# Optimization experiments

Measured on AMD Instinct MI355X. Metric: run time of the kernel, lower is better.

## Reference

```python
import jax, jax.numpy as jnp
import numpy as np

NUM_HEADS = 4
HEAD_DIM = 64
BN_EPS = 1e-5


def setup_inputs() -> dict:
    key = jax.random.key(0)
    ks = jax.random.split(key, 6)
    B, C, H, W = 8, 256, 48, 48
    HD = NUM_HEADS * HEAD_DIM  # 256
    x = jax.random.normal(ks[0], (B, C, H, W), dtype=jnp.float32)
    q_w = jax.random.normal(ks[1], (HD, C), dtype=jnp.float32) * (1.0 / np.sqrt(C))
    k_w = jax.random.normal(ks[2], (HEAD_DIM, C), dtype=jnp.float32) * (1.0 / np.sqrt(C))
    v_w = jax.random.normal(ks[3], (HEAD_DIM, C), dtype=jnp.float32) * (1.0 / np.sqrt(C))
    proj_w = jax.random.normal(ks[4], (C, HD), dtype=jnp.float32) * (1.0 / np.sqrt(HD))
    proj_b = jnp.zeros((C,), dtype=jnp.float32)
    gamma = jnp.ones((C,), dtype=jnp.float32)
    beta = jnp.zeros((C,), dtype=jnp.float32)
    return {"x": x, "q_w": q_w, "k_w": k_w, "v_w": v_w,
            "proj_w": proj_w, "proj_b": proj_b, "gamma": gamma, "beta": beta}


def reference(x, q_w, k_w, v_w, proj_w, proj_b, gamma, beta):
    B, C, H, W = x.shape
    N = H * W
    scale = HEAD_DIM ** -0.5
    xf = x.reshape(B, C, N)  # 1x1 conv == channel matmul
    q = jnp.einsum('oc,bcn->bon', q_w, xf).reshape(B, NUM_HEADS, HEAD_DIM, N)
    k = jnp.einsum('dc,bcn->bdn', k_w, xf)  # shared single KV head (MQA)
    v = jnp.einsum('dc,bcn->bdn', v_w, xf)
    # scores: [B, heads, N, N]
    attn = jnp.einsum('bhdn,bdm->bhnm', q, k) * scale
    attn = jax.nn.softmax(attn, axis=-1)
    out = jnp.einsum('bhnm,bdm->bhdn', attn, v)  # [B, heads, d, N]
    out = out.reshape(B, NUM_HEADS * HEAD_DIM, N)
    out = jnp.einsum('co,bon->bcn', proj_w, out) + proj_b[None, :, None]
    out = out.reshape(B, C, H, W)
    # BatchNorm2d (training-mode batch statistics, biased variance)
    mean = jnp.mean(out, axis=(0, 2, 3), keepdims=True)
    var = jnp.var(out, axis=(0, 2, 3), keepdims=True)
    out = gamma[None, :, None, None] * (out - mean) * jax.lax.rsqrt(var + BN_EPS) + beta[None, :, None, None]
    return out + x
```

## Files before the change

### kernel.cpp

```cpp
#include <hip/hip_runtime.h>
#include <hip/hip_bf16.h>
#include <math.h>

#define BB 8
#define CCH 256
#define NN 2304
#define NH 4
#define HDIM 64
#define QKV_ROWS 384
#define BN_EPS 1e-5f
#define NTILES 36
#define NPART 288
#define SLOG2E 0.18033688011112042f

typedef short bf16x8 __attribute__((ext_vector_type(8)));
typedef short bf16x4 __attribute__((ext_vector_type(4)));
typedef float f32x4 __attribute__((ext_vector_type(4)));

#if __has_builtin(__builtin_amdgcn_exp2f)
#define EXP2(x) __builtin_amdgcn_exp2f(x)
#else
#define EXP2(x) __expf((x) * 0.6931471805599453f)
#endif

#define MFMA32(a, b, c) __builtin_amdgcn_mfma_f32_16x16x32_bf16(a, b, c, 0, 0, 0)

__device__ __forceinline__ unsigned bfpair(float a, float b) {
    __hip_bfloat162 h = __float22bfloat162_rn(make_float2(a, b));
    return *(unsigned*)&h;
}
__device__ __forceinline__ unsigned short f2bf(float f) {
    unsigned u = __float_as_uint(f);
    u = (u + 0x7FFFu + ((u >> 16) & 1u)) >> 16;
    return (unsigned short)u;
}
__device__ __forceinline__ float bf2f(unsigned short s) {
    return __uint_as_float((unsigned)s << 16);
}

__global__ __launch_bounds__(256) void prep_k(
    const float* __restrict__ x,
    const float* __restrict__ qw, const float* __restrict__ kw,
    const float* __restrict__ vw, const float* __restrict__ pw,
    unsigned short* __restrict__ xT, unsigned short* __restrict__ xb,
    unsigned short* __restrict__ Wb, unsigned short* __restrict__ Pb)
{
    const int bid = blockIdx.x;
    const int tid = threadIdx.x;
    if (bid < 1152) {
        __shared__ float sX[64][65];
        const int b  = bid / 144;
        const int rem = bid - b * 144;
        const int nb = (rem >> 2) * 64;
        const int cb = (rem & 3) * 64;

        #pragma unroll
        for (int u = 0; u < 4; ++u) {
            int c  = (tid >> 4) + 16 * u;
            int n4 = (tid & 15) * 4;
            float4 v = *(const float4*)(x + ((size_t)(b * CCH + cb + c)) * NN + nb + n4);
            sX[c][n4+0] = v.x; sX[c][n4+1] = v.y; sX[c][n4+2] = v.z; sX[c][n4+3] = v.w;
        }
        __syncthreads();

        const int n  = tid >> 2;
        const int cg = (tid & 3) * 16;
        unsigned vals[8];
        #pragma unroll
        for (int p = 0; p < 8; ++p)
            vals[p] = bfpair(sX[cg + 2*p][n], sX[cg + 2*p + 1][n]);
        unsigned short* dst = xT + ((size_t)(b * NN + nb + n)) * CCH + cb + cg;
        *(uint4*)dst = make_uint4(vals[0], vals[1], vals[2], vals[3]);
        *(uint4*)(dst + 8) = make_uint4(vals[4], vals[5], vals[6], vals[7]);

        #pragma unroll
        for (int it = 0; it < 2; ++it) {
            int flat = tid + 256 * it;
            int row = flat >> 3;
            int n8  = (flat & 7) * 8;
            unsigned vv[4];
            #pragma unroll
            for (int p = 0; p < 4; ++p)
                vv[p] = bfpair(sX[row][n8 + 2*p], sX[row][n8 + 2*p + 1]);
            *(uint4*)(xb + ((size_t)(b * CCH + cb + row)) * NN + nb + n8) =
                make_uint4(vv[0], vv[1], vv[2], vv[3]);
        }
    } else {
        int idx = (bid - 1152) * 256 + tid;
        if (idx < 98304) {
            int o = idx >> 8, c = idx & 255;
            float v;
            if (o < 256)      v = qw[(size_t)o * CCH + c] * SLOG2E;
            else if (o < 320) v = kw[(size_t)(o - 256) * CCH + c];
            else              v = vw[(size_t)(o - 320) * CCH + c];
            Wb[idx] = f2bf(v);
        } else {
            int j = idx - 98304;
            if (j < 65536) Pb[j] = f2bf(pw[j]);
        }
    }
}

__global__ __launch_bounds__(128) void qkv_mfma_k(
    const unsigned short* __restrict__ Wb, const unsigned short* __restrict__ xT,
    unsigned short* __restrict__ Qt, unsigned short* __restrict__ Kt,
    unsigned short* __restrict__ Vn)
{
    __shared__ unsigned short sE[2][64 * 72];
    const int tid = threadIdx.x;
    const int wave = tid >> 6;
    const int lane = tid & 63;
    const int quad = lane >> 4;
    const int l15  = lane & 15;
    const int b  = blockIdx.x;
    const int nb = blockIdx.y * 64;
    const int mb = blockIdx.z * 128 + wave * 64;

    const unsigned short* Ab = Wb + (size_t)(mb + l15) * CCH + quad * 8;
    const unsigned short* Bb = xT + ((size_t)(b * NN + nb + l15)) * CCH + quad * 8;

    f32x4 C[4][4] = {};
    bf16x8 aA[2][4], bB[2][4];
    #pragma unroll
    for (int i = 0; i < 4; ++i) aA[0][i] = *(const bf16x8*)(Ab + (size_t)(16*i) * CCH);
    #pragma unroll
    for (int j = 0; j < 4; ++j) bB[0][j] = *(const bf16x8*)(Bb + (size_t)(16*j) * CCH);

    #pragma unroll
    for (int kk = 0; kk < 8; ++kk) {
        const int cur = kk & 1;
        if (kk < 7) {
            const int k1 = (kk + 1) * 32;
            #pragma unroll
            for (int i = 0; i < 4; ++i) aA[cur^1][i] = *(const bf16x8*)(Ab + (size_t)(16*i) * CCH + k1);
            #pragma unroll
            for (int j = 0; j < 4; ++j) bB[cur^1][j] = *(const bf16x8*)(Bb + (size_t)(16*j) * CCH + k1);
        }
        #pragma unroll
        for (int i = 0; i < 4; ++i)
            #pragma unroll
            for (int j = 0; j < 4; ++j)
                C[i][j] = MFMA32(aA[cur][i], bB[cur][j], C[i][j]);
    }

    unsigned short* sEw = &sE[wave][0];
    if (mb < 320) {
        #pragma unroll
        for (int i = 0; i < 4; ++i)
            #pragma unroll
            for (int j = 0; j < 4; ++j) {
                unsigned p01 = bfpair(C[i][j][0], C[i][j][1]);
                unsigned p23 = bfpair(C[i][j][2], C[i][j][3]);
                unsigned short* p = sEw + (16*j + l15) * 72 + 16*i + quad*4;
                *(unsigned*)p = p01;
                *(unsigned*)(p + 2) = p23;
            }
        if (mb < 256) {
            #pragma unroll
            for (int it = 0; it < 8; ++it) {
                int flat = lane + 64 * it;
                int row = flat >> 3;
                int o8  = (flat & 7) * 8;
                uint4 v = *(const uint4*)(sEw + row * 72 + o8);
                *(uint4*)(Qt + ((size_t)(b * NN + nb + row)) * CCH + mb + o8) = v;
            }
        } else {
            #pragma unroll
            for (int it = 0; it < 8; ++it) {
                int flat = lane + 64 * it;
                int row = flat >> 3;
                int o8  = (flat & 7) * 8;
                uint4 v = *(const uint4*)(sEw + row * 72 + o8);
                *(uint4*)(Kt + ((size_t)(b * NN + nb + row)) * 64 + o8) = v;
            }
        }
    } else {
        #pragma unroll
        for (int i = 0; i < 4; ++i)
            #pragma unroll
            for (int j = 0; j < 4; ++j) {
                unsigned p01 = bfpair(C[i][j][0], C[i][j][1]);
                unsigned p23 = bfpair(C[i][j][2], C[i][j][3]);
                unsigned short* p = sEw + (16*i + quad*4) * 72 + 16*j + l15;
                p[0]   = (unsigned short)p01;
                p[72]  = (unsigned short)(p01 >> 16);
                p[144] = (unsigned short)p23;
                p[216] = (unsigned short)(p23 >> 16);
            }
        #pragma unroll
        for (int it = 0; it < 8; ++it) {
            int flat = lane + 64 * it;
            int row = flat >> 3;
            int n8  = (flat & 7) * 8;
            uint4 v = *(const uint4*)(sEw + row * 72 + n8);
            *(uint4*)(Vn + ((size_t)(b * 64 + (mb - 320) + row)) * NN + nb + n8) = v;
        }
    }
}

__global__ __launch_bounds__(512, 8) void attn_k(
    const unsigned short* __restrict__ Qt,
    const unsigned short* __restrict__ Kt,
    const unsigned short* __restrict__ Vn,
    unsigned short* __restrict__ Ao)
{
    __shared__ __align__(16) unsigned short sKV[2 * 2 * 64 * 64];

    const int tid   = threadIdx.x;
    const int wave  = tid >> 6;
    const int lane  = tid & 63;
    const int quad  = lane >> 4;
    const int l15   = lane & 15;
    const int qslot = wave & 3;
    const int hloc  = wave >> 2;
    const int qoff  = qslot * 16;
    const int b     = blockIdx.x;
    const int nb    = blockIdx.y * 64;
    const int head  = blockIdx.z * 2 + hloc;

    const bf16x8 vone8 = {(short)0x3F80, (short)0x3F80, (short)0x3F80, (short)0x3F80,
                          (short)0x3F80, (short)0x3F80, (short)0x3F80, (short)0x3F80};

    bf16x8 bQ[2];
    const unsigned short* QtB = Qt + ((size_t)(b * NN + nb + qoff + l15)) * CCH + head * 64 + quad * 8;
    #pragma unroll
    for (int s = 0; s < 2; ++s)
        bQ[s] = *(const bf16x8*)(QtB + s * 32);

    const int srow = tid >> 3;
    const int swch = ((tid & 7) ^ (srow & 7)) * 8;
    const int krow = (srow & 3) | (((srow >> 3) & 3) << 2) | (((srow >> 2) & 1) << 4) | (srow & 32);
    const int kwch = ((tid & 7) ^ (krow & 7)) * 8;
    const int sgc8 = (tid & 7) * 8;

    bf16x8 pf[2];
    pf[0] = *(const bf16x8*)(Kt + ((size_t)(b * NN + srow)) * 64 + sgc8);
    pf[1] = *(const bf16x8*)(Vn + ((size_t)(b * 64 + srow)) * NN + sgc8);
    *(bf16x8*)(sKV + 0 * 4096 + krow * 64 + kwch) = pf[0];
    *(bf16x8*)(sKV + 1 * 4096 + srow * 64 + swch) = pf[1];
    pf[0] = *(const bf16x8*)(Kt + ((size_t)(b * NN + 64 + srow)) * 64 + sgc8);
    pf[1] = *(const bf16x8*)(Vn + ((size_t)(b * 64 + srow)) * NN + 64 + sgc8);

    f32x4 O[4] = {};
    f32x4 dacc = {};

    for (int step = 0; step < NTILES; ++step) {
        const int cur = step & 1;
        __syncthreads();

        if (step + 1 < NTILES) {
            unsigned short* dstb = sKV + (cur ^ 1) * 8192;
            *(bf16x8*)(dstb + 0 * 4096 + krow * 64 + kwch) = pf[0];
            *(bf16x8*)(dstb + 1 * 4096 + srow * 64 + swch) = pf[1];
        }
        if (step + 2 < NTILES) {
            const int keys0 = (step + 2) * 64;
            pf[0] = *(const bf16x8*)(Kt + ((size_t)(b * NN + keys0 + srow)) * 64 + sgc8);
            pf[1] = *(const bf16x8*)(Vn + ((size_t)(b * 64 + srow)) * NN + keys0 + sgc8);
        }

        const unsigned short* sKb = sKV + cur * 8192;
        const unsigned short* sVb = sKb + 4096;

        f32x4 C[4] = {};
        #pragma unroll
        for (int s = 0; s < 2; ++s)
            #pragma unroll
            for (int kt = 0; kt < 4; ++kt) {
                const int row = 16*kt + l15;
                const int chsw = ((s*4 + quad) ^ (row & 7)) * 8;
                bf16x8 aK = *(const bf16x8*)(sKb + row * 64 + chsw);
                C[kt] = MFMA32(aK, bQ[s], C[kt]);
            }

        bf16x8 bP[2];
        #pragma unroll
        for (int kt2 = 0; kt2 < 2; ++kt2) {
            union { unsigned u[4]; bf16x8 v; } xp;
            const f32x4 c0 = C[2*kt2];
            const f32x4 c1 = C[2*kt2+1];
            xp.u[0] = bfpair(EXP2(c0[0]), EXP2(c0[1]));
            xp.u[1] = bfpair(EXP2(c0[2]), EXP2(c0[3]));
            xp.u[2] = bfpair(EXP2(c1[0]), EXP2(c1[1]));
            xp.u[3] = bfpair(EXP2(c1[2]), EXP2(c1[3]));
            bP[kt2] = xp.v;
        }

        dacc = MFMA32(vone8, bP[0], dacc);
        dacc = MFMA32(vone8, bP[1], dacc);

        #pragma unroll
        for (int jd = 0; jd < 4; ++jd)
            #pragma unroll
            for (int kt2 = 0; kt2 < 2; ++kt2) {
                const int row = 16*jd + l15;
                const int chsw = ((4*kt2 + quad) ^ (row & 7)) * 8;
                bf16x8 aV = *(const bf16x8*)(sVb + row * 64 + chsw);
                O[jd] = MFMA32(aV, bP[kt2], O[jd]);
            }
    }
    __syncthreads();

    const float rinv = 1.0f / dacc[0];
    unsigned short* sT = (unsigned short*)sKV;
    #pragma unroll
    for (int jd = 0; jd < 4; ++jd) {
        unsigned lo = bfpair(O[jd][0] * rinv, O[jd][1] * rinv);
        unsigned hi = bfpair(O[jd][2] * rinv, O[jd][3] * rinv);
        *(uint2*)(sT + (hloc * 64 + qoff + l15) * 72 + 16*jd + quad*4) = make_uint2(lo, hi);
    }
    __syncthreads();

    #pragma unroll
    for (int it = 0; it < 2; ++it) {
        int flat = tid + 512 * it;
        int hh   = flat >> 9;
        int row  = (flat >> 3) & 63;
        int c8   = (flat & 7) * 8;
        uint4 v = *(const uint4*)(sT + (hh * 64 + row) * 72 + c8);
        *(uint4*)(Ao + ((size_t)(b * NN + nb + row)) * CCH + (blockIdx.z * 2 + hh) * 64 + c8) = v;
    }
}

__global__ __launch_bounds__(128) void proj_mfma_k(
    const unsigned short* __restrict__ Pb, const unsigned short* __restrict__ Ao,
    const float* __restrict__ pb, unsigned short* __restrict__ projb,
    float* __restrict__ psum, float* __restrict__ psq)
{
    __shared__ unsigned short sE[2][64 * 72];
    const int tid = threadIdx.x;
    const int wave = tid >> 6;
    const int lane = tid & 63;
    const int quad = lane >> 4;
    const int l15  = lane & 15;
    const int b  = blockIdx.x;
    const int nb = blockIdx.y * 64;
    const int mb = blockIdx.z * 128 + wave * 64;
    const int part = b * NTILES + blockIdx.y;

    const unsigned short* Ab = Pb + (size_t)(mb + l15) * CCH + quad * 8;
    const unsigned short* Bb = Ao + ((size_t)(b * NN + nb + l15)) * CCH + quad * 8;

    f32x4 C[4][4] = {};
    bf16x8 aA[2][4], bB[2][4];
    #pragma unroll
    for (int i = 0; i < 4; ++i) aA[0][i] = *(const bf16x8*)(Ab + (size_t)(16*i) * CCH);
    #pragma unroll
    for (int j = 0; j < 4; ++j) bB[0][j] = *(const bf16x8*)(Bb + (size_t)(16*j) * CCH);

    #pragma unroll
    for (int kk = 0; kk < 8; ++kk) {
        const int cur = kk & 1;
        if (kk < 7) {
            const int k1 = (kk + 1) * 32;
            #pragma unroll
            for (int i = 0; i < 4; ++i) aA[cur^1][i] = *(const bf16x8*)(Ab + (size_t)(16*i) * CCH + k1);
            #pragma unroll
            for (int j = 0; j < 4; ++j) bB[cur^1][j] = *(const bf16x8*)(Bb + (size_t)(16*j) * CCH + k1);
        }
        #pragma unroll
        for (int i = 0; i < 4; ++i)
            #pragma unroll
            for (int j = 0; j < 4; ++j)
                C[i][j] = MFMA32(aA[cur][i], bB[cur][j], C[i][j]);
    }

    unsigned short* sEw = &sE[wave][0];
    #pragma unroll
    for (int i = 0; i < 4; ++i) {
        #pragma unroll
        for (int r = 0; r < 4; ++r) {
            const int ch = mb + 16*i + quad*4 + r;
            const float bias = pb[ch];
            float v0 = C[i][0][r] + bias, v1 = C[i][1][r] + bias;
            float v2 = C[i][2][r] + bias, v3 = C[i][3][r] + bias;
            C[i][0][r] = v0; C[i][1][r] = v1; C[i][2][r] = v2; C[i][3][r] = v3;
            float rs = (v0 + v1) + (v2 + v3);
            float rq = (v0*v0 + v1*v1) + (v2*v2 + v3*v3);
            rs += __shfl_xor(rs, 1); rq += __shfl_xor(rq, 1);
            rs += __shfl_xor(rs, 2); rq += __shfl_xor(rq, 2);
            rs += __shfl_xor(rs, 4); rq += __shfl_xor(rq, 4);
            rs += __shfl_xor(rs, 8); rq += __shfl_xor(rq, 8);
            if (l15 == 0) {
                psum[(size_t)ch * NPART + part] = rs;
                psq [(size_t)ch * NPART + part] = rq;
            }
        }
    }

    #pragma unroll
    for (int i = 0; i < 4; ++i)
        #pragma unroll
        for (int j = 0; j < 4; ++j) {
            unsigned p01 = bfpair(C[i][j][0], C[i][j][1]);
            unsigned p23 = bfpair(C[i][j][2], C[i][j][3]);
            unsigned short* p = sEw + (16*i + quad*4) * 72 + 16*j + l15;
            p[0]   = (unsigned short)p01;
            p[72]  = (unsigned short)(p01 >> 16);
            p[144] = (unsigned short)p23;
            p[216] = (unsigned short)(p23 >> 16);
        }
    #pragma unroll
    for (int it = 0; it < 8; ++it) {
        int flat = lane + 64 * it;
        int row = flat >> 3;
        int n8  = (flat & 7) * 8;
        uint4 v = *(const uint4*)(sEw + row * 72 + n8);
        *(uint4*)(projb + ((size_t)(b * CCH + mb + row)) * NN + nb + n8) = v;
    }
}

__global__ __launch_bounds__(256) void bn_apply_k(
    const unsigned short* __restrict__ projb, const unsigned short* __restrict__ xb,
    const float* __restrict__ psum, const float* __restrict__ psq,
    const float* __restrict__ gamma, const float* __restrict__ beta,
    float* __restrict__ out)
{
    const int tid = threadIdx.x;
    const int b = blockIdx.x;
    const int c = blockIdx.y;

    float s = 0.f, q = 0.f;
    for (int k = tid; k < NPART; k += 256) {
        s += psum[(size_t)c * NPART + k];
        q += psq [(size_t)c * NPART + k];
    }
    __shared__ float rs[256], rq[256];
    rs[tid] = s; rq[tid] = q;
    __syncthreads();
    for (int off = 128; off > 0; off >>= 1) {
        if (tid < off) { rs[tid] += rs[tid + off]; rq[tid] += rq[tid + off]; }
        __syncthreads();
    }
    const float inv_n = 1.0f / (float)(BB * NN);
    float mean = rs[0] * inv_n;
    float var  = rq[0] * inv_n - mean * mean;
    float scv = gamma[c] * rsqrtf(var + BN_EPS);
    float shv = beta[c] - mean * scv;

    #pragma unroll
    for (int it = 0; it < 2; ++it) {
        int chunk = tid + 256 * it;
        if (chunk < 288) {
            size_t base = ((size_t)(b * CCH + c)) * NN + chunk * 8;
            uint4 pv = *(const uint4*)(projb + base);
            uint4 xv = *(const uint4*)(xb + base);
            const unsigned short* pp = (const unsigned short*)&pv;
            const unsigned short* xx = (const unsigned short*)&xv;
            float4 r0, r1;
            r0.x = scv * bf2f(pp[0]) + shv + bf2f(xx[0]);
            r0.y = scv * bf2f(pp[1]) + shv + bf2f(xx[1]);
            r0.z = scv * bf2f(pp[2]) + shv + bf2f(xx[2]);
            r0.w = scv * bf2f(pp[3]) + shv + bf2f(xx[3]);
            r1.x = scv * bf2f(pp[4]) + shv + bf2f(xx[4]);
            r1.y = scv * bf2f(pp[5]) + shv + bf2f(xx[5]);
            r1.z = scv * bf2f(pp[6]) + shv + bf2f(xx[6]);
            r1.w = scv * bf2f(pp[7]) + shv + bf2f(xx[7]);
            *(float4*)(out + base) = r0;
            *(float4*)(out + base + 4) = r1;
        }
    }
}

extern "C" void kernel_launch(void* const* d_in, const int* in_sizes, int n_in,
                              void* d_out, int out_size, void* d_ws, size_t ws_size,
                              hipStream_t stream)
{
    const float* x     = (const float*)d_in[0];
    const float* qw    = (const float*)d_in[1];
    const float* kw    = (const float*)d_in[2];
    const float* vw    = (const float*)d_in[3];
    const float* pw    = (const float*)d_in[4];
    const float* pb    = (const float*)d_in[5];
    const float* gamma = (const float*)d_in[6];
    const float* beta  = (const float*)d_in[7];
    float* out = (float*)d_out;

    char* ws = (char*)d_ws;
    unsigned short* xT = (unsigned short*)ws;
    unsigned short* Ao = (unsigned short*)ws;
    unsigned short* Wb = (unsigned short*)(ws + 9437184);
    unsigned short* Pb = (unsigned short*)(ws + 9633792);
    unsigned short* Qt = (unsigned short*)(ws + 9764864);
    unsigned short* Kt = (unsigned short*)(ws + 19202048);
    unsigned short* Vn = (unsigned short*)(ws + 21561344);
    unsigned short* projb = (unsigned short*)(ws + 9764864);
    float* psum  = (float*)(ws + 28639232);
    float* psq   = (float*)(ws + 28934144);
    unsigned short* xb = (unsigned short*)(ws + 29229056);

    prep_k<<<1792, 256, 0, stream>>>(x, qw, kw, vw, pw, xT, xb, Wb, Pb);

    dim3 g1(BB, NN / 64, 3);
    qkv_mfma_k<<<g1, 128, 0, stream>>>(Wb, xT, Qt, Kt, Vn);

    dim3 g2(BB, NN / 64, NH / 2);
    attn_k<<<g2, 512, 0, stream>>>(Qt, Kt, Vn, Ao);

    dim3 g3(BB, NN / 64, 2);
    proj_mfma_k<<<g3, 128, 0, stream>>>(Pb, Ao, pb, projb, psum, psq);

    dim3 g4(BB, CCH);
    bn_apply_k<<<g4, 256, 0, stream>>>(projb, xb, psum, psq, gamma, beta, out);
}
```

Baseline: 198.6 us.

## Give each attention wave two query tiles to reuse K/V fragments

```diff
diff --git a/kernel.cpp b/kernel.cpp
--- a/kernel.cpp
+++ b/kernel.cpp
@@ -198,7 +198,7 @@
     }
 }
 
-__global__ __launch_bounds__(512, 8) void attn_k(
+__global__ __launch_bounds__(256, 4) void attn_k(
     const unsigned short* __restrict__ Qt,
     const unsigned short* __restrict__ Kt,
     const unsigned short* __restrict__ Vn,
@@ -211,38 +211,47 @@
     const int lane  = tid & 63;
     const int quad  = lane >> 4;
     const int l15   = lane & 15;
-    const int qslot = wave & 3;
-    const int hloc  = wave >> 2;
-    const int qoff  = qslot * 16;
+    const int qoff  = wave * 32;
     const int b     = blockIdx.x;
-    const int nb    = blockIdx.y * 64;
-    const int head  = blockIdx.z * 2 + hloc;
+    const int nb    = blockIdx.y * 128;
+    const int head  = blockIdx.z;
 
     const bf16x8 vone8 = {(short)0x3F80, (short)0x3F80, (short)0x3F80, (short)0x3F80,
                           (short)0x3F80, (short)0x3F80, (short)0x3F80, (short)0x3F80};
 
-    bf16x8 bQ[2];
+    bf16x8 bQ[2][2];
     const unsigned short* QtB = Qt + ((size_t)(b * NN + nb + qoff + l15)) * CCH + head * 64 + quad * 8;
     #pragma unroll
-    for (int s = 0; s < 2; ++s)
-        bQ[s] = *(const bf16x8*)(QtB + s * 32);
-
-    const int srow = tid >> 3;
-    const int swch = ((tid & 7) ^ (srow & 7)) * 8;
-    const int krow = (srow & 3) | (((srow >> 3) & 3) << 2) | (((srow >> 2) & 1) << 4) | (srow & 32);
-    const int kwch = ((tid & 7) ^ (krow & 7)) * 8;
-    const int sgc8 = (tid & 7) * 8;
-
-    bf16x8 pf[2];
-    pf[0] = *(const bf16x8*)(Kt + ((size_t)(b * NN + srow)) * 64 + sgc8);
-    pf[1] = *(const bf16x8*)(Vn + ((size_t)(b * 64 + srow)) * NN + sgc8);
-    *(bf16x8*)(sKV + 0 * 4096 + krow * 64 + kwch) = pf[0];
-    *(bf16x8*)(sKV + 1 * 4096 + srow * 64 + swch) = pf[1];
-    pf[0] = *(const bf16x8*)(Kt + ((size_t)(b * NN + 64 + srow)) * 64 + sgc8);
-    pf[1] = *(const bf16x8*)(Vn + ((size_t)(b * 64 + srow)) * NN + 64 + sgc8);
-
-    f32x4 O[4] = {};
-    f32x4 dacc = {};
+    for (int qt = 0; qt < 2; ++qt)
+        #pragma unroll
+        for (int s = 0; s < 2; ++s)
+            bQ[qt][s] = *(const bf16x8*)(QtB + (size_t)(16*qt) * CCH + s * 32);
+
+    const int r0  = tid >> 3;
+    const int c8  = (tid & 7) * 8;
+    const int kr0 = (r0 & 3) | (((r0 >> 3) & 3) << 2) | (((r0 >> 2) & 1) << 4);
+    const int kwc = ((tid & 7) ^ (kr0 & 7)) * 8;
+    const int vwc = ((tid & 7) ^ (r0 & 7)) * 8;
+
+    const unsigned short* Kb = Kt + ((size_t)(b * NN + r0)) * 64 + c8;
+    const unsigned short* Vb = Vn + ((size_t)(b * 64 + r0)) * NN + c8;
+
+    bf16x8 pf[4];
+    pf[0] = *(const bf16x8*)(Kb);
+    pf[1] = *(const bf16x8*)(Kb + (size_t)32 * 64);
+    pf[2] = *(const bf16x8*)(Vb);
+    pf[3] = *(const bf16x8*)(Vb + (size_t)32 * NN);
+    *(bf16x8*)(sKV + kr0 * 64 + kwc)          = pf[0];
+    *(bf16x8*)(sKV + (kr0 + 32) * 64 + kwc)   = pf[1];
+    *(bf16x8*)(sKV + 4096 + r0 * 64 + vwc)    = pf[2];
+    *(bf16x8*)(sKV + 4096 + (r0 + 32) * 64 + vwc) = pf[3];
+    pf[0] = *(const bf16x8*)(Kb + (size_t)64 * 64);
+    pf[1] = *(const bf16x8*)(Kb + (size_t)96 * 64);
+    pf[2] = *(const bf16x8*)(Vb + 64);
+    pf[3] = *(const bf16x8*)(Vb + (size_t)32 * NN + 64);
+
+    f32x4 O[4][2] = {};
+    f32x4 dacc[2] = {};
 
     for (int step = 0; step < NTILES; ++step) {
         const int cur = step & 1;
@@ -250,19 +259,23 @@
 
         if (step + 1 < NTILES) {
             unsigned short* dstb = sKV + (cur ^ 1) * 8192;
-            *(bf16x8*)(dstb + 0 * 4096 + krow * 64 + kwch) = pf[0];
-            *(bf16x8*)(dstb + 1 * 4096 + srow * 64 + swch) = pf[1];
+            *(bf16x8*)(dstb + kr0 * 64 + kwc)             = pf[0];
+            *(bf16x8*)(dstb + (kr0 + 32) * 64 + kwc)      = pf[1];
+            *(bf16x8*)(dstb + 4096 + r0 * 64 + vwc)       = pf[2];
+            *(bf16x8*)(dstb + 4096 + (r0 + 32) * 64 + vwc) = pf[3];
         }
         if (step + 2 < NTILES) {
             const int keys0 = (step + 2) * 64;
-            pf[0] = *(const bf16x8*)(Kt + ((size_t)(b * NN + keys0 + srow)) * 64 + sgc8);
-            pf[1] = *(const bf16x8*)(Vn + ((size_t)(b * 64 + srow)) * NN + keys0 + sgc8);
+            pf[0] = *(const bf16x8*)(Kb + (size_t)keys0 * 64);
+            pf[1] = *(const bf16x8*)(Kb + (size_t)(keys0 + 32) * 64);
+            pf[2] = *(const bf16x8*)(Vb + keys0);
+            pf[3] = *(const bf16x8*)(Vb + (size_t)32 * NN + keys0);
         }
 
         const unsigned short* sKb = sKV + cur * 8192;
         const unsigned short* sVb = sKb + 4096;
 
-        f32x4 C[4] = {};
+        f32x4 C[4][2] = {};
         #pragma unroll
         for (int s = 0; s < 2; ++s)
             #pragma unroll
@@ -270,24 +283,30 @@
                 const int row = 16*kt + l15;
                 const int chsw = ((s*4 + quad) ^ (row & 7)) * 8;
                 bf16x8 aK = *(const bf16x8*)(sKb + row * 64 + chsw);
-                C[kt] = MFMA32(aK, bQ[s], C[kt]);
-            }
-
-        bf16x8 bP[2];
+                C[kt][0] = MFMA32(aK, bQ[0][s], C[kt][0]);
+                C[kt][1] = MFMA32(aK, bQ[1][s], C[kt][1]);
+            }
+
+        bf16x8 bP[2][2];
+        #pragma unroll
+        for (int kt2 = 0; kt2 < 2; ++kt2)
+            #pragma unroll
+            for (int qt = 0; qt < 2; ++qt) {
+                union { unsigned u[4]; bf16x8 v; } xp;
+                const f32x4 c0 = C[2*kt2][qt];
+                const f32x4 c1 = C[2*kt2+1][qt];
+                xp.u[0] = bfpair(EXP2(c0[0]), EXP2(c0[1]));
+                xp.u[1] = bfpair(EXP2(c0[2]), EXP2(c0[3]));
+                xp.u[2] = bfpair(EXP2(c1[0]), EXP2(c1[1]));
+                xp.u[3] = bfpair(EXP2(c1[2]), EXP2(c1[3]));
+                bP[kt2][qt] = xp.v;
+            }
+
         #pragma unroll
         for (int kt2 = 0; kt2 < 2; ++kt2) {
-            union { unsigned u[4]; bf16x8 v; } xp;
-            const f32x4 c0 = C[2*kt2];
-            const f32x4 c1 = C[2*kt2+1];
-            xp.u[0] = bfpair(EXP2(c0[0]), EXP2(c0[1]));
-            xp.u[1] = bfpair(EXP2(c0[2]), EXP2(c0[3]));
-            xp.u[2] = bfpair(EXP2(c1[0]), EXP2(c1[1]));
-            xp.u[3] = bfpair(EXP2(c1[2]), EXP2(c1[3]));
-            bP[kt2] = xp.v;
-        }
-
-        dacc = MFMA32(vone8, bP[0], dacc);
-        dacc = MFMA32(vone8, bP[1], dacc);
+            dacc[0] = MFMA32(vone8, bP[kt2][0], dacc[0]);
+            dacc[1] = MFMA32(vone8, bP[kt2][1], dacc[1]);
+        }
 
         #pragma unroll
         for (int jd = 0; jd < 4; ++jd)
@@ -296,29 +315,33 @@
                 const int row = 16*jd + l15;
                 const int chsw = ((4*kt2 + quad) ^ (row & 7)) * 8;
                 bf16x8 aV = *(const bf16x8*)(sVb + row * 64 + chsw);
-                O[jd] = MFMA32(aV, bP[kt2], O[jd]);
+                O[jd][0] = MFMA32(aV, bP[kt2][0], O[jd][0]);
+                O[jd][1] = MFMA32(aV, bP[kt2][1], O[jd][1]);
             }
     }
     __syncthreads();
 
-    const float rinv = 1.0f / dacc[0];
+    float rinv[2];
+    rinv[0] = 1.0f / dacc[0][0];
+    rinv[1] = 1.0f / dacc[1][0];
     unsigned short* sT = (unsigned short*)sKV;
     #pragma unroll
-    for (int jd = 0; jd < 4; ++jd) {
-        unsigned lo = bfpair(O[jd][0] * rinv, O[jd][1] * rinv);
-        unsigned hi = bfpair(O[jd][2] * rinv, O[jd][3] * rinv);
-        *(uint2*)(sT + (hloc * 64 + qoff + l15) * 72 + 16*jd + quad*4) = make_uint2(lo, hi);
-    }
+    for (int qt = 0; qt < 2; ++qt)
+        #pragma unroll
+        for (int jd = 0; jd < 4; ++jd) {
+            unsigned lo = bfpair(O[jd][qt][0] * rinv[qt], O[jd][qt][1] * rinv[qt]);
+            unsigned hi = bfpair(O[jd][qt][2] * rinv[qt], O[jd][qt][3] * rinv[qt]);
+            *(uint2*)(sT + (qoff + 16*qt + l15) * 72 + 16*jd + quad*4) = make_uint2(lo, hi);
+        }
     __syncthreads();
 
     #pragma unroll
-    for (int it = 0; it < 2; ++it) {
-        int flat = tid + 512 * it;
-        int hh   = flat >> 9;
-        int row  = (flat >> 3) & 63;
-        int c8   = (flat & 7) * 8;
-        uint4 v = *(const uint4*)(sT + (hh * 64 + row) * 72 + c8);
-        *(uint4*)(Ao + ((size_t)(b * NN + nb + row)) * CCH + (blockIdx.z * 2 + hh) * 64 + c8) = v;
+    for (int it = 0; it < 4; ++it) {
+        int flat = tid + 256 * it;
+        int row  = flat >> 3;
+        int cc8  = (flat & 7) * 8;
+        uint4 v = *(const uint4*)(sT + row * 72 + cc8);
+        *(uint4*)(Ao + ((size_t)(b * NN + nb + row)) * CCH + head * 64 + cc8) = v;
     }
 }
 
@@ -494,8 +517,8 @@
     dim3 g1(BB, NN / 64, 3);
     qkv_mfma_k<<<g1, 128, 0, stream>>>(Wb, xT, Qt, Kt, Vn);
 
-    dim3 g2(BB, NN / 64, NH / 2);
-    attn_k<<<g2, 512, 0, stream>>>(Qt, Kt, Vn, Ao);
+    dim3 g2(BB, NN / 128, NH);
+    attn_k<<<g2, 256, 0, stream>>>(Qt, Kt, Vn, Ao);
 
     dim3 g3(BB, NN / 64, 2);
     proj_mfma_k<<<g3, 128, 0, stream>>>(Pb, Ao, pb, projb, psum, psq);
```

Measured after the change: 193.6 us. 2.5% less time.
